# Optimization experiments

Hardware: AMD Instinct MI355X
Metric: run time of the kernel (lower is better)

Reference implementation:

```python
import jax, jax.numpy as jnp
import numpy as np

BSZ, DIM, TSZ = 8, 512, 2048
STEPS, NNEG, OFFSET = 12, 10, 1
COPIES = NNEG + 1


def setup_inputs() -> dict:
    key = jax.random.key(0)
    k1, k2, k3, k4, k5 = jax.random.split(key, 5)
    x = jax.random.normal(k1, (BSZ, DIM, TSZ), dtype=jnp.float32)
    y = jax.random.normal(k2, (BSZ, DIM, TSZ), dtype=jnp.float32)
    # ConvTranspose2d(in, out, (1, steps)) on width-1 input == per-step linear maps
    W = jax.random.normal(k3, (DIM, DIM, STEPS), dtype=jnp.float32) * 0.02
    b = jax.random.normal(k4, (DIM,), dtype=jnp.float32) * 0.02
    # negative indices, faithful to torch sample_negatives (within-utterance)
    tszs = jnp.repeat(jnp.arange(TSZ, dtype=jnp.int32), NNEG)  # [TSZ*NNEG]
    neg = jax.random.randint(k5, (BSZ, NNEG * TSZ), 0, TSZ - 1, dtype=jnp.int32)
    neg = neg + (neg >= tszs[None, :]).astype(jnp.int32)  # avoid self
    neg = neg + (jnp.arange(BSZ, dtype=jnp.int32) * TSZ)[:, None]  # per-batch offset
    return {"x": x, "y": y, "W": W, "b": b, "neg_idxs": neg}


def reference(x, y, W, b, neg_idxs):
    bsz, dim, tsz = y.shape
    # project_to_steps: [B, D, T] -> [B, D, T, STEPS]
    xp = jnp.einsum('bit,iok->botk', x, W) + b[None, :, None, None]
    # sample negatives: gather from flattened [D, B*T]
    y_flat = jnp.transpose(y, (1, 0, 2)).reshape(dim, bsz * tsz)
    negs = y_flat[:, neg_idxs.reshape(-1)]
    negs = negs.reshape(dim, bsz, NNEG, tsz).transpose(2, 1, 0, 3)  # [NNEG,B,D,T]
    targets = jnp.concatenate([y[None], negs], axis=0)  # [COPIES,B,D,T]
    steps = min(STEPS, tsz - OFFSET)
    segs = []
    for i in range(steps):
        off = i + OFFSET
        # [T-off, B, COPIES]
        s = jnp.einsum('bct,nbct->tbn', xp[:, :, : tsz - off, i], targets[:, :, :, off:])
        segs.append(s.reshape(-1))
    predictions = jnp.concatenate(segs).reshape(-1, COPIES)  # infonce view
    labels = jnp.zeros((predictions.shape[0],), dtype=jnp.int32)
    return predictions, labels
```

## Files before the change

kernel.cpp:

```cpp
#include <hip/hip_runtime.h>

#define BSZ 8
#define DIM 512
#define TSZ 2048
#define STEPS 12
#define NNEG 10
#define COPIES 11
#define TCH 64
#define GTCH 128

typedef unsigned short ushortT;
typedef unsigned int uintT;
typedef __attribute__((ext_vector_type(8))) short short8v;
typedef __attribute__((ext_vector_type(4))) float f32x4;

#define AS1 __attribute__((address_space(1)))
#define AS3 __attribute__((address_space(3)))

#define XP_OFF 39845888ull
#define WS_NEEDED (XP_OFF + 201326592ull)

__device__ __forceinline__ ushortT f2bf(float f) {
    uintT u = __builtin_bit_cast(uintT, f);
    u = (u + 0x7fffu + ((u >> 16) & 1u)) >> 16;
    return (ushortT)u;
}

__global__ __launch_bounds__(1024) void transpose_xy_kernel(const float* __restrict__ x,
                                                            const float* __restrict__ y,
                                                            ushortT* __restrict__ xt,
                                                            ushortT* __restrict__ yt) {
    __shared__ float tile[32][33];
    const int z = blockIdx.z;
    const int bb = z & 7;
    const float* src = (z < 8) ? x : y;
    ushortT* dst = (z < 8) ? xt : yt;
    const int d0 = blockIdx.y * 32;
    const int t0 = blockIdx.x * 32;
    const int tx = threadIdx.x, ty = threadIdx.y;
    tile[ty][tx] = src[((size_t)(bb * DIM + d0 + ty)) * TSZ + t0 + tx];
    __syncthreads();
    dst[((size_t)(bb * TSZ + t0 + ty)) * DIM + d0 + tx] = f2bf(tile[tx][ty]);
}

__global__ __launch_bounds__(256) void transpose_w_kernel(const float* __restrict__ W,
                                                          ushortT* __restrict__ Wco) {
    __shared__ float buf[DIM * STEPS];
    const int d = blockIdx.x;
    for (int idx = threadIdx.x; idx < DIM * STEPS; idx += 256)
        buf[idx] = W[(size_t)d * DIM * STEPS + idx];
    __syncthreads();
    for (int idx = threadIdx.x; idx < DIM * STEPS; idx += 256) {
        const int i = idx >> 9;
        const int c = idx & 511;
        Wco[((size_t)i * DIM + c) * DIM + d] = f2bf(buf[c * STEPS + i]);
    }
}

__global__ __launch_bounds__(1024, 4) void gemm_kernel(const ushortT* __restrict__ xt,
                                                       const ushortT* __restrict__ Wco,
                                                       const float* __restrict__ bias,
                                                       ushortT* __restrict__ xp) {
    __shared__ ushortT xs[GTCH * 256];
    const int id = blockIdx.x;
    const int i = id % 12;
    const int rest = id / 12;
    const int tchunk = rest & 15;
    const int bb = rest >> 4;
    const int t0 = tchunk * GTCH;
    const int tid = threadIdx.x;
    const int lane = tid & 63;
    const int w = tid >> 6;
    const int r16 = lane & 15;
    const int g = lane >> 4;

    const ushortT* gbase = xt + ((size_t)bb * TSZ + t0) * DIM;
    const ushortT* wbase = Wco + (size_t)i * DIM * DIM + (size_t)(w * 32 + r16) * DIM + 8 * g;
    f32x4 acc[8][2] = {};

    #pragma unroll
    for (int kh = 0; kh < 2; ++kh) {
        #pragma unroll
        for (int p = 0; p < 4; ++p) {
            const int chunk = p * 1024 + tid;
            const int row = chunk >> 5;
            const int cl = chunk & 31;
            const int csrc = cl ^ (row & 7);
            __builtin_amdgcn_global_load_lds(
                (const AS1 uintT*)(gbase + (size_t)row * DIM + kh * 256 + csrc * 8),
                (AS3 uintT*)(&xs[chunk * 8]), 16, 0, 0);
        }
        __syncthreads();

        #pragma unroll
        for (int kt8 = 0; kt8 < 8; ++kt8) {
            const int kt = kh * 8 + kt8;
            short8v af[2];
            #pragma unroll
            for (int cc = 0; cc < 2; ++cc)
                af[cc] = *(const short8v*)(wbase + (size_t)cc * 16 * DIM + kt * 32);
            #pragma unroll
            for (int t4 = 0; t4 < 8; ++t4) {
                const int row = t4 * 16 + r16;
                const int cidx = (kt8 * 4 + g) ^ (row & 7);
                const short8v bfr = *(const short8v*)(&xs[row * 256 + cidx * 8]);
                acc[t4][0] = __builtin_amdgcn_mfma_f32_16x16x32_bf16(af[0], bfr, acc[t4][0], 0, 0, 0);
                acc[t4][1] = __builtin_amdgcn_mfma_f32_16x16x32_bf16(af[1], bfr, acc[t4][1], 0, 0, 0);
            }
        }
        __syncthreads();
    }

    ushortT* xrow = xp + (((size_t)bb * STEPS + i) * TSZ + t0) * DIM;
    #pragma unroll
    for (int cc = 0; cc < 2; ++cc) {
        const int c0 = w * 32 + cc * 16 + 4 * g;
        const float4 bv = *(const float4*)(bias + c0);
        #pragma unroll
        for (int t4 = 0; t4 < 8; ++t4) {
            const f32x4 v = acc[t4][cc];
            ushort4 h;
            h.x = f2bf(v[0] + bv.x);
            h.y = f2bf(v[1] + bv.y);
            h.z = f2bf(v[2] + bv.z);
            h.w = f2bf(v[3] + bv.w);
            *(ushort4*)(xrow + (size_t)(t4 * 16 + r16) * DIM + c0) = h;
        }
    }
}

#define STAGE_PRED(buf, ii)                                                          \
    {                                                                                \
        const int offp = (ii) + 1;                                                   \
        const ushortT* srcp = xpb + (size_t)(ii) * TSZ * DIM;                        \
        for (int c = tid; c < 1024; c += 768) {                                      \
            const int row = c >> 6;                                                  \
            const int cl = c & 63;                                                   \
            const int csrc = cl ^ (row & 7);                                         \
            const int rt = max(tau0 - offp + row, 0);                                \
            __builtin_amdgcn_global_load_lds(                                        \
                (const AS1 uintT*)(srcp + (size_t)rt * DIM + csrc * 8),              \
                (AS3 uintT*)(&as[buf][c * 8]), 16, 0, 0);                            \
        }                                                                            \
    }

__global__ __launch_bounds__(768, 2) void predict_kernel(const ushortT* __restrict__ xp,
                                                         const ushortT* __restrict__ yt,
                                                         const int* __restrict__ neg,
                                                         float* __restrict__ out) {
    __shared__ ushortT as[2][16 * DIM];
    const int id = blockIdx.x;
    const int bb = id & 7;
    const int tau0 = (id >> 3) * 16;
    const int tid = threadIdx.x;
    const int lane = tid & 63;
    const int w = tid >> 6;
    const int r16 = lane & 15;
    const int g = lane >> 4;
    const int n = w;
    const int tau = tau0 + r16;
    const bool active = (n < COPIES);
    const bool isdiag = (g == (r16 >> 2));
    const int treg = r16 & 3;

    short8v bf[16];
    if (active) {
        const int col = (n == 0) ? (bb * TSZ + tau)
                                 : neg[bb * (NNEG * TSZ) + (n - 1) * TSZ + tau];
        const ushortT* bp = yt + (size_t)col * DIM + g * 8;
        #pragma unroll
        for (int kt = 0; kt < 16; ++kt) bf[kt] = *(const short8v*)(bp + kt * 32);
    }

    const ushortT* xpb = xp + ((size_t)bb * STEPS) * (size_t)TSZ * DIM;

    STAGE_PRED(0, 0)
    __syncthreads();

    for (int i = 0; i < STEPS; ++i) {
        const int cur = i & 1;
        if (i + 1 < STEPS) STAGE_PRED(cur ^ 1, i + 1)

        if (active) {
            f32x4 pacc = {};
            #pragma unroll
            for (int kt = 0; kt < 16; ++kt) {
                const short8v af = *(const short8v*)(&as[cur][r16 * DIM + (((kt * 4 + g) ^ (r16 & 7)) << 3)]);
                pacc = __builtin_amdgcn_mfma_f32_16x16x32_bf16(af, bf[kt], pacc, 0, 0, 0);
            }
            const int t = tau - (i + 1);
            if (isdiag && t >= 0) {
                const size_t segoff = 88ull * (2047ull * (size_t)i - (size_t)(i * (i - 1)) / 2);
                const float v01 = (treg & 1) ? pacc[1] : pacc[0];
                const float v23 = (treg & 1) ? pacc[3] : pacc[2];
                const float v = (treg & 2) ? v23 : v01;
                out[segoff + ((size_t)t * BSZ + bb) * COPIES + n] = v;
            }
        }
        __syncthreads();
    }
}

__global__ __launch_bounds__(512, 4) void fused_kernel(const ushortT* __restrict__ xt,
                                                       const ushortT* __restrict__ yt,
                                                       const ushortT* __restrict__ Wco,
                                                       const float* __restrict__ bias,
                                                       const int* __restrict__ neg,
                                                       float* __restrict__ out) {
    __shared__ ushortT xs[TCH * DIM];
    const int id = blockIdx.x;
    const int bb = id & 7;
    const int id2 = id >> 3;
    const int i = id2 % 12;
    const int tchunk = id2 / 12;
    const int t0 = tchunk * TCH;
    const int tid = threadIdx.x;
    const int lane = tid & 63;
    const int w = tid >> 6;
    const int r16 = lane & 15;
    const int g = lane >> 4;

    {
        const ushortT* gbase = xt + ((size_t)bb * TSZ + t0) * DIM;
        #pragma unroll
        for (int p = 0; p < 8; ++p) {
            const int chunk = p * 512 + tid;
            const int row = chunk >> 6;
            const int cl = chunk & 63;
            const int csrc = cl ^ (row & 7);
            __builtin_amdgcn_global_load_lds(
                (const AS1 uintT*)(gbase + (size_t)row * DIM + csrc * 8),
                (AS3 uintT*)(&xs[chunk * 8]), 16, 0, 0);
        }
    }
    __syncthreads();

    f32x4 acc[4][4] = {};
    const ushortT* wbase = Wco + (size_t)i * DIM * DIM + (size_t)(w * 64 + r16) * DIM + 8 * g;
    #pragma unroll 2
    for (int kt = 0; kt < 16; ++kt) {
        short8v bfr[4];
        #pragma unroll
        for (int t4 = 0; t4 < 4; ++t4) {
            const int row = t4 * 16 + r16;
            bfr[t4] = *(const short8v*)(&xs[row * DIM + (((kt * 4 + g) ^ (row & 7)) << 3)]);
        }
        #pragma unroll
        for (int cc = 0; cc < 4; ++cc) {
            const short8v af = *(const short8v*)(wbase + (size_t)cc * 16 * DIM + kt * 32);
            #pragma unroll
            for (int t4 = 0; t4 < 4; ++t4)
                acc[t4][cc] = __builtin_amdgcn_mfma_f32_16x16x32_bf16(af, bfr[t4], acc[t4][cc], 0, 0, 0);
        }
    }
    __syncthreads();

    #pragma unroll
    for (int cc = 0; cc < 4; ++cc) {
        const int c0 = w * 64 + cc * 16 + 4 * g;
        const float4 bv = *(const float4*)(bias + c0);
        #pragma unroll
        for (int t4 = 0; t4 < 4; ++t4) {
            const f32x4 v = acc[t4][cc];
            ushort4 h;
            h.x = f2bf(v[0] + bv.x);
            h.y = f2bf(v[1] + bv.y);
            h.z = f2bf(v[2] + bv.z);
            h.w = f2bf(v[3] + bv.w);
            const int tloc = t4 * 16 + r16;
            const int pchunk = ((c0 >> 3) ^ (tloc & 7));
            *(ushort4*)(&xs[tloc * DIM + (pchunk << 3) + (g & 1) * 4]) = h;
        }
    }
    __syncthreads();

    const int off = i + 1;
    const int tlim = TSZ - off;
    const size_t segoff = 88ull * (2047ull * (size_t)i - (size_t)(i * (i - 1)) / 2);
    const int tt = w & 3;
    const int t00 = tt * 16;
    const int nbase = (w >> 2) * 5;
    const int arow = t00 + r16;
    const int tb = t0 + t00 + r16;
    const int tauc = min(tb + off, TSZ - 1);
    const bool isdiag = (g == (r16 >> 2));
    const int treg = r16 & 3;

    const ushortT* bptrs[6];
    #pragma unroll
    for (int nj = 0; nj < 6; ++nj) {
        const int nn = nbase + nj;
        const int col = (nn == 0) ? (bb * TSZ + tauc)
                                  : neg[bb * (NNEG * TSZ) + (nn - 1) * TSZ + tauc];
        bptrs[nj] = yt + (size_t)col * DIM + g * 8;
    }

    f32x4 pacc[6] = {};
    #pragma unroll
    for (int kt = 0; kt < 16; ++kt) {
        const short8v af = *(const short8v*)(&xs[arow * DIM + (((kt * 4 + g) ^ (arow & 7)) << 3)]);
        #pragma unroll
        for (int nj = 0; nj < 6; ++nj) {
            const short8v bfv = *(const short8v*)(bptrs[nj] + kt * 32);
            pacc[nj] = __builtin_amdgcn_mfma_f32_16x16x32_bf16(af, bfv, pacc[nj], 0, 0, 0);
        }
    }

    if (isdiag && tb < tlim) {
        #pragma unroll
        for (int nj = 0; nj < 6; ++nj) {
            const float v01 = (treg & 1) ? pacc[nj][1] : pacc[nj][0];
            const float v23 = (treg & 1) ? pacc[nj][3] : pacc[nj][2];
            const float v = (treg & 2) ? v23 : v01;
            out[segoff + ((size_t)tb * BSZ + bb) * COPIES + (nbase + nj)] = v;
        }
    }
}

__global__ __launch_bounds__(256) void labels_kernel(float* __restrict__ out) {
    const int idx = blockIdx.x * 256 + threadIdx.x;
    if (idx < 195984) out[2155824 + idx] = 0.0f;
}

extern "C" void kernel_launch(void* const* d_in, const int* in_sizes, int n_in,
                              void* d_out, int out_size, void* d_ws, size_t ws_size,
                              hipStream_t stream) {
    const float* x = (const float*)d_in[0];
    const float* y = (const float*)d_in[1];
    const float* W = (const float*)d_in[2];
    const float* b = (const float*)d_in[3];
    const int* neg = (const int*)d_in[4];
    float* out = (float*)d_out;
    ushortT* xt = (ushortT*)d_ws;
    ushortT* yt = (ushortT*)((char*)d_ws + 16777216);
    ushortT* Wco = (ushortT*)((char*)d_ws + 33554432);

    transpose_xy_kernel<<<dim3(TSZ / 32, DIM / 32, 16), dim3(32, 32), 0, stream>>>(x, y, xt, yt);
    transpose_w_kernel<<<dim3(DIM), dim3(256), 0, stream>>>(W, Wco);

    if (ws_size >= WS_NEEDED) {
        ushortT* xp = (ushortT*)((char*)d_ws + XP_OFF);
        gemm_kernel<<<dim3(BSZ * STEPS * (TSZ / GTCH)), dim3(1024), 0, stream>>>(xt, Wco, b, xp);
        predict_kernel<<<dim3(BSZ * (TSZ / 16)), dim3(768), 0, stream>>>(xp, yt, neg, out);
    } else {
        fused_kernel<<<dim3(BSZ * STEPS * (TSZ / TCH)), dim3(512), 0, stream>>>(xt, yt, Wco, b, neg, out);
    }
    labels_kernel<<<dim3(766), dim3(256), 0, stream>>>(out);
}
```

Measured before the change: 300.8 us.

## Double-buffer GEMM LDS staging over four K-quarters to overlap loads and MFMA

The projection GEMM now stages the x tile into LDS in four 128-wide K quarters using two ping-pong buffers, instead of two 256-wide halves in a single buffer. The next quarter's global-to-LDS load is issued before computing the current one. The aim is to hide global load latency behind MFMA work rather than stalling at each barrier. Total LDS use stays the same, but there are more barriers, and the overlap depends on how the compiler places waitcnt before each barrier.

Result: slower. 393.3 us (+30.8%).

```diff
diff --git a/kernel.cpp b/kernel.cpp
--- a/kernel.cpp
+++ b/kernel.cpp
@@ -61,7 +61,7 @@
                                                        const ushortT* __restrict__ Wco,
                                                        const float* __restrict__ bias,
                                                        ushortT* __restrict__ xp) {
-    __shared__ ushortT xs[GTCH * 256];
+    __shared__ ushortT xs[2][GTCH * 128];
     const int id = blockIdx.x;
     const int i = id % 12;
     const int rest = id / 12;
@@ -78,23 +78,29 @@
     const ushortT* wbase = Wco + (size_t)i * DIM * DIM + (size_t)(w * 32 + r16) * DIM + 8 * g;
     f32x4 acc[8][2] = {};
 
-    #pragma unroll
-    for (int kh = 0; kh < 2; ++kh) {
-        #pragma unroll
-        for (int p = 0; p < 4; ++p) {
-            const int chunk = p * 1024 + tid;
-            const int row = chunk >> 5;
-            const int cl = chunk & 31;
-            const int csrc = cl ^ (row & 7);
-            __builtin_amdgcn_global_load_lds(
-                (const AS1 uintT*)(gbase + (size_t)row * DIM + kh * 256 + csrc * 8),
-                (AS3 uintT*)(&xs[chunk * 8]), 16, 0, 0);
-        }
-        __syncthreads();
-
-        #pragma unroll
-        for (int kt8 = 0; kt8 < 8; ++kt8) {
-            const int kt = kh * 8 + kt8;
+#define STAGE_G(buf, q)                                                              \
+    {                                                                                \
+        _Pragma("unroll")                                                            \
+        for (int p = 0; p < 2; ++p) {                                                \
+            const int c2 = p * 1024 + tid;                    \
+            const int row = c2 >> 4;               \
+            const int cl = c2 & 15;                                                  \
+            const int csrc = cl ^ (row & 7);                                         \
+            __builtin_amdgcn_global_load_lds(                                        \
+                (const AS1 uintT*)(gbase + (size_t)row * DIM + (q) * 128 + csrc * 8),\
+                (AS3 uintT*)(&xs[buf][c2 * 8]), 16, 0, 0);                           \
+        }                                                                            \
+    }
+
+    STAGE_G(0, 0)
+    __syncthreads();
+
+    #pragma unroll
+    for (int q = 0; q < 4; ++q) {
+        if (q + 1 < 4) STAGE_G((q + 1) & 1, q + 1)
+        #pragma unroll
+        for (int kq = 0; kq < 4; ++kq) {
+            const int kt = q * 4 + kq;
             short8v af[2];
             #pragma unroll
             for (int cc = 0; cc < 2; ++cc)
@@ -102,14 +108,15 @@
             #pragma unroll
             for (int t4 = 0; t4 < 8; ++t4) {
                 const int row = t4 * 16 + r16;
-                const int cidx = (kt8 * 4 + g) ^ (row & 7);
-                const short8v bfr = *(const short8v*)(&xs[row * 256 + cidx * 8]);
+                const int cidx = (kq * 4 + g) ^ (row & 7);
+                const short8v bfr = *(const short8v*)(&xs[q & 1][row * 128 + cidx * 8]);
                 acc[t4][0] = __builtin_amdgcn_mfma_f32_16x16x32_bf16(af[0], bfr, acc[t4][0], 0, 0, 0);
                 acc[t4][1] = __builtin_amdgcn_mfma_f32_16x16x32_bf16(af[1], bfr, acc[t4][1], 0, 0, 0);
             }
         }
         __syncthreads();
     }
+#undef STAGE_G
 
     ushortT* xrow = xp + (((size_t)bb * STEPS + i) * TSZ + t0) * DIM;
     #pragma unroll
```

## Stage two steps per barrier in predict kernel and remap gemm block order

Applied to the files above, without the earlier changes.

The predict kernel now stages the projected rows for two steps at once into a doubled shared buffer. This halves the number of loop iterations and __syncthreads barriers, from 12 to 6, and issues more async global-to-LDS loads per stage. The gemm kernel's block-index decode is also reordered so that 8 consecutive blocks cover different time chunks or batches of the same step, which changes L2 locality for W. LDS use per block doubles to 64KB, which may limit occupancy at 2 blocks per CU.

Result: faster. 289.1 us (-3.9%).

```diff
diff --git a/kernel.cpp b/kernel.cpp
--- a/kernel.cpp
+++ b/kernel.cpp
@@ -63,10 +63,13 @@
                                                        ushortT* __restrict__ xp) {
     __shared__ ushortT xs[GTCH * 256];
     const int id = blockIdx.x;
-    const int i = id % 12;
-    const int rest = id / 12;
-    const int tchunk = rest & 15;
-    const int bb = rest >> 4;
+    const int low = id & 7;
+    const int m = id >> 3;
+    const int i = m % 12;
+    const int gh = m / 12;
+    const int g2 = gh * 8 + low;
+    const int tchunk = g2 & 15;
+    const int bb = g2 >> 4;
     const int t0 = tchunk * GTCH;
     const int tid = threadIdx.x;
     const int lane = tid & 63;
@@ -129,18 +132,20 @@
     }
 }
 
-#define STAGE_PRED(buf, ii)                                                          \
+#define STAGE_PRED2(buf, rr)                                                         \
     {                                                                                \
-        const int offp = (ii) + 1;                                                   \
-        const ushortT* srcp = xpb + (size_t)(ii) * TSZ * DIM;                        \
-        for (int c = tid; c < 1024; c += 768) {                                      \
-            const int row = c >> 6;                                                  \
-            const int cl = c & 63;                                                   \
+        for (int c = tid; c < 2048; c += 768) {                                      \
+            const int sub = c >> 10;                                                 \
+            const int ii = (rr) * 2 + sub;                                           \
+            const int offp = ii + 1;                                                 \
+            const int cc2 = c & 1023;                                                \
+            const int row = cc2 >> 6;                                                \
+            const int cl = cc2 & 63;                                                 \
             const int csrc = cl ^ (row & 7);                                         \
             const int rt = max(tau0 - offp + row, 0);                                \
             __builtin_amdgcn_global_load_lds(                                        \
-                (const AS1 uintT*)(srcp + (size_t)rt * DIM + csrc * 8),              \
-                (AS3 uintT*)(&as[buf][c * 8]), 16, 0, 0);                            \
+                (const AS1 uintT*)(xpb + (size_t)ii * TSZ * DIM + (size_t)rt * DIM + csrc * 8), \
+                (AS3 uintT*)(&as[buf][sub][cc2 * 8]), 16, 0, 0);                     \
         }                                                                            \
     }
 
@@ -148,7 +153,7 @@
                                                          const ushortT* __restrict__ yt,
                                                          const int* __restrict__ neg,
                                                          float* __restrict__ out) {
-    __shared__ ushortT as[2][16 * DIM];
+    __shared__ ushortT as[2][2][16 * DIM];
     const int id = blockIdx.x;
     const int bb = id & 7;
     const int tau0 = (id >> 3) * 16;
@@ -174,27 +179,31 @@
 
     const ushortT* xpb = xp + ((size_t)bb * STEPS) * (size_t)TSZ * DIM;
 
-    STAGE_PRED(0, 0)
-    __syncthreads();
-
-    for (int i = 0; i < STEPS; ++i) {
-        const int cur = i & 1;
-        if (i + 1 < STEPS) STAGE_PRED(cur ^ 1, i + 1)
-
-        if (active) {
-            f32x4 pacc = {};
-            #pragma unroll
-            for (int kt = 0; kt < 16; ++kt) {
-                const short8v af = *(const short8v*)(&as[cur][r16 * DIM + (((kt * 4 + g) ^ (r16 & 7)) << 3)]);
-                pacc = __builtin_amdgcn_mfma_f32_16x16x32_bf16(af, bf[kt], pacc, 0, 0, 0);
-            }
-            const int t = tau - (i + 1);
-            if (isdiag && t >= 0) {
-                const size_t segoff = 88ull * (2047ull * (size_t)i - (size_t)(i * (i - 1)) / 2);
-                const float v01 = (treg & 1) ? pacc[1] : pacc[0];
-                const float v23 = (treg & 1) ? pacc[3] : pacc[2];
-                const float v = (treg & 2) ? v23 : v01;
-                out[segoff + ((size_t)t * BSZ + bb) * COPIES + n] = v;
+    STAGE_PRED2(0, 0)
+    __syncthreads();
+
+    for (int r = 0; r < 6; ++r) {
+        const int cur = r & 1;
+        if (r + 1 < 6) STAGE_PRED2(cur ^ 1, r + 1)
+
+        #pragma unroll
+        for (int sub = 0; sub < 2; ++sub) {
+            const int i = r * 2 + sub;
+            if (active) {
+                f32x4 pacc = {};
+                #pragma unroll
+                for (int kt = 0; kt < 16; ++kt) {
+                    const short8v af = *(const short8v*)(&as[cur][sub][r16 * DIM + (((kt * 4 + g) ^ (r16 & 7)) << 3)]);
+                    pacc = __builtin_amdgcn_mfma_f32_16x16x32_bf16(af, bf[kt], pacc, 0, 0, 0);
+                }
+                const int t = tau - (i + 1);
+                if (isdiag && t >= 0) {
+                    const size_t segoff = 88ull * (2047ull * (size_t)i - (size_t)(i * (i - 1)) / 2);
+                    const float v01 = (treg & 1) ? pacc[1] : pacc[0];
+                    const float v23 = (treg & 1) ? pacc[3] : pacc[2];
+                    const float v = (treg & 2) ? v23 : v01;
+                    out[segoff + ((size_t)t * BSZ + bb) * COPIES + n] = v;
+                }
             }
         }
         __syncthreads();
```

## Deepen predict-kernel LDS staging to eight step buffers and remap GEMM block order

Applied to the files above, without the earlier changes.

The predict kernel now stages eight steps of projected rows into LDS at once, then computes in batches of four with only three barriers, instead of double-buffering one step at a time with a barrier per step. This cuts the number of sync points and gives more loads in flight to hide global latency. LDS use rises from 32KB to 128KB per block, which may lower occupancy below the two blocks per CU the launch bounds target. The GEMM kernel also reorders its block-id decode so eight consecutive blocks share a step index, which should improve cache reuse of the weight slice.

Result: faster. 290.3 us (-3.5%).

```diff
diff --git a/kernel.cpp b/kernel.cpp
--- a/kernel.cpp
+++ b/kernel.cpp
@@ -63,10 +63,13 @@
                                                        ushortT* __restrict__ xp) {
     __shared__ ushortT xs[GTCH * 256];
     const int id = blockIdx.x;
-    const int i = id % 12;
-    const int rest = id / 12;
-    const int tchunk = rest & 15;
-    const int bb = rest >> 4;
+    const int low = id & 7;
+    const int m = id >> 3;
+    const int i = m % 12;
+    const int gh = m / 12;
+    const int g2 = gh * 8 + low;
+    const int tchunk = g2 & 15;
+    const int bb = g2 >> 4;
     const int t0 = tchunk * GTCH;
     const int tid = threadIdx.x;
     const int lane = tid & 63;
@@ -129,7 +132,7 @@
     }
 }
 
-#define STAGE_PRED(buf, ii)                                                          \
+#define STAGE_SUB(sbuf, ii)                                                          \
     {                                                                                \
         const int offp = (ii) + 1;                                                   \
         const ushortT* srcp = xpb + (size_t)(ii) * TSZ * DIM;                        \
@@ -140,7 +143,25 @@
             const int rt = max(tau0 - offp + row, 0);                                \
             __builtin_amdgcn_global_load_lds(                                        \
                 (const AS1 uintT*)(srcp + (size_t)rt * DIM + csrc * 8),              \
-                (AS3 uintT*)(&as[buf][c * 8]), 16, 0, 0);                            \
+                (AS3 uintT*)(&as[sbuf][c * 8]), 16, 0, 0);                           \
+        }                                                                            \
+    }
+
+#define COMPUTE_SUB(sbuf, ii)                                                        \
+    if (active) {                                                                    \
+        f32x4 pacc = {};                                                             \
+        _Pragma("unroll")                                                            \
+        for (int kt = 0; kt < 16; ++kt) {                                            \
+            const short8v af = *(const short8v*)(&as[sbuf][r16 * DIM + (((kt * 4 + g) ^ (r16 & 7)) << 3)]); \
+            pacc = __builtin_amdgcn_mfma_f32_16x16x32_bf16(af, bf[kt], pacc, 0, 0, 0); \
+        }                                                                            \
+        const int t = tau - ((ii) + 1);                                              \
+        if (isdiag && t >= 0) {                                                      \
+            const size_t segoff = 88ull * (2047ull * (size_t)(ii) - (size_t)((ii) * ((ii) - 1)) / 2); \
+            const float v01 = (treg & 1) ? pacc[1] : pacc[0];                        \
+            const float v23 = (treg & 1) ? pacc[3] : pacc[2];                        \
+            const float v = (treg & 2) ? v23 : v01;                                  \
+            out[segoff + ((size_t)t * BSZ + bb) * COPIES + n] = v;                   \
         }                                                                            \
     }
 
@@ -148,7 +169,7 @@
                                                          const ushortT* __restrict__ yt,
                                                          const int* __restrict__ neg,
                                                          float* __restrict__ out) {
-    __shared__ ushortT as[2][16 * DIM];
+    __shared__ ushortT as[8][16 * DIM];
     const int id = blockIdx.x;
     const int bb = id & 7;
     const int tau0 = (id >> 3) * 16;
@@ -174,31 +195,22 @@
 
     const ushortT* xpb = xp + ((size_t)bb * STEPS) * (size_t)TSZ * DIM;
 
-    STAGE_PRED(0, 0)
-    __syncthreads();
-
-    for (int i = 0; i < STEPS; ++i) {
-        const int cur = i & 1;
-        if (i + 1 < STEPS) STAGE_PRED(cur ^ 1, i + 1)
-
-        if (active) {
-            f32x4 pacc = {};
-            #pragma unroll
-            for (int kt = 0; kt < 16; ++kt) {
-                const short8v af = *(const short8v*)(&as[cur][r16 * DIM + (((kt * 4 + g) ^ (r16 & 7)) << 3)]);
-                pacc = __builtin_amdgcn_mfma_f32_16x16x32_bf16(af, bf[kt], pacc, 0, 0, 0);
-            }
-            const int t = tau - (i + 1);
-            if (isdiag && t >= 0) {
-                const size_t segoff = 88ull * (2047ull * (size_t)i - (size_t)(i * (i - 1)) / 2);
-                const float v01 = (treg & 1) ? pacc[1] : pacc[0];
-                const float v23 = (treg & 1) ? pacc[3] : pacc[2];
-                const float v = (treg & 2) ? v23 : v01;
-                out[segoff + ((size_t)t * BSZ + bb) * COPIES + n] = v;
-            }
-        }
-        __syncthreads();
-    }
+    #pragma unroll
+    for (int s = 0; s < 8; ++s) STAGE_SUB(s, s)
+    __syncthreads();
+
+    #pragma unroll
+    for (int s = 0; s < 4; ++s) COMPUTE_SUB(s, s)
+    __syncthreads();
+
+    #pragma unroll
+    for (int s = 0; s < 4; ++s) STAGE_SUB(s, s + 8)
+    #pragma unroll
+    for (int s = 4; s < 8; ++s) COMPUTE_SUB(s, s)
+    __syncthreads();
+
+    #pragma unroll
+    for (int s = 0; s < 4; ++s) COMPUTE_SUB(s, s + 8)
 }
 
 __global__ __launch_bounds__(512, 4) void fused_kernel(const ushortT* __restrict__ xt,
```
